# Performance work log

Measured on AMD Instinct MI355X. Metric: run time of the kernel, lower is better.

The kernel has to match this reference:

```python
import jax, jax.numpy as jnp
import numpy as np

G, S, P = 128, 32, 16          # graphs, subgraphs per graph, nodes per subgraph
D, C, NH, OUT = 768, 256, 4, 7 # input dim, hidden dim, GAT heads, classes


def setup_inputs() -> dict:
    key = jax.random.key(0)
    ks = jax.random.split(key, 17)
    n = lambda k, shape, s=0.05: jax.random.normal(k, shape, dtype=jnp.float32) * s
    return {
        "x": jax.random.normal(ks[0], (G, S, P, D), dtype=jnp.float32),
        # GATConv(768 -> 256, heads=4, concat=False): lin weight, att vectors, bias
        "gat_W": n(ks[1], (D, NH * C)),
        "att_src": n(ks[2], (NH, C)),
        "att_dst": n(ks[3], (NH, C)),
        "gat_b": n(ks[4], (C,)),
        # GRU(256 -> 256), torch layout [3*H, in]
        "gru_Wih": n(ks[5], (3 * C, C)),
        "gru_Whh": n(ks[6], (3 * C, C)),
        "gru_bih": n(ks[7], (3 * C,)),
        "gru_bhh": n(ks[8], (3 * C,)),
        # scale_up_projection Linear(256 -> 768)
        "up_W": n(ks[9], (D, C)),
        "up_b": n(ks[10], (D,)),
        # speaker_projection Linear(1536 -> 768) + ReLU
        "sp_W": n(ks[11], (D, 2 * D)),
        "sp_b": n(ks[12], (D,)),
        # GlobalAttention gate Linear(256 -> 1)
        "att_W": n(ks[13], (1, C)),
        "att_b": n(ks[14], (1,)),
        # classifier Linear(256 -> 7)
        "cls_W": n(ks[15], (OUT, C)),
        "cls_b": n(ks[16], (OUT,)),
    }


def _gat(x, W, a_src, a_dst, b):
    # PyG GATConv on a star graph (speaker = local node 0 -> all others) with
    # default add_self_loops=True, negative_slope=0.2, concat=False (mean over heads).
    # x: [G, P, D]
    h = jnp.einsum('gpd,dhc->gphc', x, W.reshape(D, NH, C))     # per-head transform
    es = jnp.sum(h * a_src, -1)                                 # [G, P, NH]
    ed = jnp.sum(h * a_dst, -1)
    lrelu = lambda v: jnp.where(v > 0, v, 0.2 * v)
    e_spk = lrelu(es[:, :1] + ed)   # edge speaker -> t
    e_slf = lrelu(es + ed)          # self loop t -> t
    w = jax.nn.softmax(jnp.stack([e_spk, e_slf], -1), axis=-1)  # [G, P, NH, 2]
    # for t == 0 both terms are h[:,0] and weights sum to 1, matching the
    # speaker node receiving only its self loop.
    out = w[..., 0:1] * h[:, :1] + w[..., 1:2] * h              # [G, P, NH, C]
    return out.mean(axis=2) + b


def _gru_cell(xin, h, Wih, Whh, bih, bhh):
    gi = xin @ Wih.T + bih
    gh = h @ Whh.T + bhh
    ir, iz, inn = jnp.split(gi, 3, -1)
    hr, hz, hn = jnp.split(gh, 3, -1)
    r = jax.nn.sigmoid(ir + hr)
    z = jax.nn.sigmoid(iz + hz)
    return (1 - z) * jnp.tanh(inn + r * hn) + z * h


def _forward(x, gat_W, att_src, att_dst, gat_b, gru_Wih, gru_Whh, gru_bih, gru_bhh,
             up_W, up_b, sp_W, sp_b, att_W, att_b, cls_W, cls_b):
    g, s, p, d = x.shape
    m0 = _gat(x[:, 0], gat_W, att_src, att_dst, gat_b)  # [G, P, C]
    h0 = jnp.zeros((g, p, C), x.dtype)

    def step(carry, _):
        h_run, m_prev = carry
        # running GRU hidden over memory prefix, then one zero-input step
        # (equivalent to rerunning the GRU over [m_0..m_{j-1}, 0])
        h_run = _gru_cell(m_prev, h_run, gru_Wih, gru_Whh, gru_bih, gru_bhh)
        h_nxt = _gru_cell(jnp.zeros_like(h_run), h_run, gru_Wih, gru_Whh, gru_bih, gru_bhh)
        pooled = h_nxt @ up_W.T + up_b                  # [G, P, D]
        # faithful to source: non_speaker_indices covers ALL nodes (torch.equal
        # shape-mismatch bug), and speaker_info is read AFTER the overwrite,
        # so the speaker concat is [pooled, pooled] and raw x[:, j>=1] is unused.
        spk = jnp.concatenate([pooled[:, 0], pooled[:, 0]], -1)  # [G, 2D]
        spk = jax.nn.relu(spk @ sp_W.T + sp_b)
        x_new = pooled.at[:, 0].set(spk)
        m = _gat(x_new, gat_W, att_src, att_dst, gat_b)
        return (h_run, m), m

    (_, _), ms = jax.lax.scan(step, (h0, m0), None, length=s - 1)
    mem = jnp.concatenate([m0[None], ms], axis=0)        # [S, G, P, C]
    # GlobalAttention pool over the P nodes of each subgraph memory state
    gate = jax.nn.softmax(jnp.squeeze(mem @ att_W.T + att_b, -1), axis=-1)  # [S, G, P]
    pooled = jnp.einsum('sgp,sgpc->sgc', gate, mem)
    logits = pooled @ cls_W.T + cls_b                    # [S, G, OUT]
    # torch stacks graph-major: [G*S, 1, OUT]
    return jnp.transpose(logits, (1, 0, 2)).reshape(g * s, 1, OUT)


def reference(x, gat_W, att_src, att_dst, gat_b, gru_Wih, gru_Whh, gru_bih, gru_bhh,
              up_W, up_b, sp_W, sp_b, att_W, att_b, cls_W, cls_b):
    return _forward(x, gat_W, att_src, att_dst, gat_b, gru_Wih, gru_Whh, gru_bih,
                    gru_bhh, up_W, up_b, sp_W, sp_b, att_W, att_b, cls_W, cls_b)
```

## Files before the change

### kernel.cpp

```cpp
#include <hip/hip_runtime.h>
#include <math.h>

#define NG 128
#define NS 32
#define NP 16
#define ND 768
#define NC 256
#define NHD 4
#define NOUT 7
#define NR 2048

typedef unsigned short ushortT;
typedef short bf16x8 __attribute__((ext_vector_type(8)));
typedef float f32x4 __attribute__((ext_vector_type(4)));

__device__ __forceinline__ ushortT f2b(float f) {
    union { float f; unsigned u; } v; v.f = f;
    unsigned r = (v.u + 0x7FFF + ((v.u >> 16) & 1)) >> 16;
    return (ushortT)r;
}
__device__ __forceinline__ float sigf(float v) { return 1.f / (1.f + expf(-v)); }

#define MFMA16(a, b, c) __builtin_amdgcn_mfma_f32_16x16x32_bf16((a), (b), (c), 0, 0, 0)

__global__ __launch_bounds__(256) void bgemm_kernel(
    const ushortT* __restrict__ A, const ushortT* __restrict__ Asub,
    const ushortT* __restrict__ Bt, const float* __restrict__ bias,
    float* __restrict__ outF, ushortT* __restrict__ outH,
    int N, int K, int act)
{
    __shared__ short As[64 * 40];
    __shared__ short Bs[64 * 40];
    const int tid = threadIdx.x;
    const int lane = tid & 63, wid = tid >> 6;
    const int quad = lane >> 4, l15 = lane & 15;
    const int row0 = blockIdx.y * 64, col0 = blockIdx.x * 64;
    const int mh = (wid & 1) * 32, nh = (wid >> 1) * 32;
    const int sr = tid >> 2, skq = (tid & 3) * 8;
    const int grow_s = row0 + sr;
    const ushortT* aptr = (Asub && ((grow_s & 15) == 0))
        ? Asub + (size_t)(grow_s >> 4) * K : A + (size_t)grow_s * K;
    const ushortT* bptr = Bt + (size_t)(col0 + sr) * K;

    f32x4 acc[2][2];
    for (int i = 0; i < 2; ++i)
        for (int j = 0; j < 2; ++j) acc[i][j] = (f32x4){0.f, 0.f, 0.f, 0.f};

    for (int kk = 0; kk < K; kk += 32) {
        __syncthreads();
        *(uint4*)&As[sr * 40 + skq] = *(const uint4*)(aptr + kk + skq);
        *(uint4*)&Bs[sr * 40 + skq] = *(const uint4*)(bptr + kk + skq);
        __syncthreads();
        bf16x8 af0 = *(const bf16x8*)&As[(mh + l15) * 40 + quad * 8];
        bf16x8 af1 = *(const bf16x8*)&As[(mh + 16 + l15) * 40 + quad * 8];
        bf16x8 bf0 = *(const bf16x8*)&Bs[(nh + l15) * 40 + quad * 8];
        bf16x8 bf1 = *(const bf16x8*)&Bs[(nh + 16 + l15) * 40 + quad * 8];
        acc[0][0] = MFMA16(af0, bf0, acc[0][0]);
        acc[0][1] = MFMA16(af0, bf1, acc[0][1]);
        acc[1][0] = MFMA16(af1, bf0, acc[1][0]);
        acc[1][1] = MFMA16(af1, bf1, acc[1][1]);
    }
#pragma unroll
    for (int mt = 0; mt < 2; ++mt)
#pragma unroll
        for (int nt = 0; nt < 2; ++nt) {
            const int gc = col0 + nh + nt * 16 + l15;
            const float bv = bias ? bias[gc] : 0.f;
#pragma unroll
            for (int r = 0; r < 4; ++r) {
                const int gr = row0 + mh + mt * 16 + quad * 4 + r;
                float v = acc[mt][nt][r] + bv;
                if (act) v = fmaxf(v, 0.f);
                if (outF) outF[(size_t)gr * N + gc] = v;
                if (outH) outH[(size_t)gr * N + gc] = f2b(v);
            }
        }
}

__global__ __launch_bounds__(256) void gru1_mfma_kernel(
    const ushortT* __restrict__ mB, const ushortT* __restrict__ hB,
    const ushortT* __restrict__ WihB, const ushortT* __restrict__ WhhB,
    const float* __restrict__ bih, const float* __restrict__ bhh,
    float* __restrict__ hF, ushortT* __restrict__ hBout)
{
    __shared__ short As[2 * 32 * 264];
    __shared__ short Bs[384 * 40];
    const int tid = threadIdx.x;
    const int lane = tid & 63, wid = tid >> 6;
    const int quad = lane >> 4, l15 = lane & 15;
    const int row0 = blockIdx.y * 32;
    const int n0 = blockIdx.x * 64;
    const int mt = wid & 1, nhh = (wid >> 1) * 32;

    for (int c = tid; c < 2048; c += 256) {
        const int mat = c >> 10, r2 = c & 1023, row = r2 >> 5, kc = (r2 & 31) * 8;
        const ushortT* src = (mat ? hB : mB) + (size_t)(row0 + row) * NC + kc;
        *(uint4*)&As[mat * 8448 + row * 264 + kc] = *(const uint4*)src;
    }
    f32x4 acc[2][3][2];
    for (int w = 0; w < 2; ++w)
        for (int g = 0; g < 3; ++g)
            for (int n = 0; n < 2; ++n) acc[w][g][n] = (f32x4){0.f, 0.f, 0.f, 0.f};

    for (int kk = 0; kk < 256; kk += 32) {
        __syncthreads();
        for (int c = tid; c < 1536; c += 256) {
            const int j = c >> 2, kq = (c & 3) * 8;
            const int w = j / 192, j2 = j - w * 192, gt = j2 >> 6, nloc = j2 & 63;
            const ushortT* src = (w ? WhhB : WihB) +
                (size_t)(gt * 256 + n0 + nloc) * NC + kk + kq;
            *(uint4*)&Bs[j * 40 + kq] = *(const uint4*)src;
        }
        __syncthreads();
        bf16x8 af0 = *(const bf16x8*)&As[(mt * 16 + l15) * 264 + kk + quad * 8];
        bf16x8 af1 = *(const bf16x8*)&As[8448 + (mt * 16 + l15) * 264 + kk + quad * 8];
#pragma unroll
        for (int gt = 0; gt < 3; ++gt)
#pragma unroll
            for (int nt = 0; nt < 2; ++nt) {
                const int jb = gt * 64 + nhh + nt * 16 + l15;
                bf16x8 b0 = *(const bf16x8*)&Bs[jb * 40 + quad * 8];
                bf16x8 b1 = *(const bf16x8*)&Bs[(192 + jb) * 40 + quad * 8];
                acc[0][gt][nt] = MFMA16(af0, b0, acc[0][gt][nt]);
                acc[1][gt][nt] = MFMA16(af1, b1, acc[1][gt][nt]);
            }
    }
#pragma unroll
    for (int nt = 0; nt < 2; ++nt) {
        const int c = n0 + nhh + nt * 16 + l15;
        const float br = bih[c], bz = bih[256 + c], bn = bih[512 + c];
        const float cr = bhh[c], cz = bhh[256 + c], cn = bhh[512 + c];
#pragma unroll
        for (int r = 0; r < 4; ++r) {
            const int grow = row0 + mt * 16 + quad * 4 + r;
            const size_t idx = (size_t)grow * NC + c;
            const float hold = hF[idx];
            const float rg = sigf(acc[0][0][nt][r] + br + acc[1][0][nt][r] + cr);
            const float zg = sigf(acc[0][1][nt][r] + bz + acc[1][1][nt][r] + cz);
            const float ng = tanhf(acc[0][2][nt][r] + bn + rg * (acc[1][2][nt][r] + cn));
            const float hn = (1.f - zg) * ng + zg * hold;
            hF[idx] = hn;
            hBout[idx] = f2b(hn);
        }
    }
}

__global__ __launch_bounds__(256) void gru2_mfma_kernel(
    const ushortT* __restrict__ hB, const ushortT* __restrict__ WhhB,
    const float* __restrict__ bih, const float* __restrict__ bhh,
    const float* __restrict__ hF, ushortT* __restrict__ hnB,
    ushortT* __restrict__ h0c)
{
    __shared__ short As[32 * 264];
    __shared__ short Bs[192 * 40];
    const int tid = threadIdx.x;
    const int lane = tid & 63, wid = tid >> 6;
    const int quad = lane >> 4, l15 = lane & 15;
    const int row0 = blockIdx.y * 32;
    const int n0 = blockIdx.x * 64;
    const int mt = wid & 1, nhh = (wid >> 1) * 32;

    for (int c = tid; c < 1024; c += 256) {
        const int row = c >> 5, kc = (c & 31) * 8;
        *(uint4*)&As[row * 264 + kc] =
            *(const uint4*)(hB + (size_t)(row0 + row) * NC + kc);
    }
    f32x4 acc[3][2];
    for (int g = 0; g < 3; ++g)
        for (int n = 0; n < 2; ++n) acc[g][n] = (f32x4){0.f, 0.f, 0.f, 0.f};

    for (int kk = 0; kk < 256; kk += 32) {
        __syncthreads();
        for (int c = tid; c < 768; c += 256) {
            const int j = c >> 2, kq = (c & 3) * 8;
            const int gt = j >> 6, nloc = j & 63;
            *(uint4*)&Bs[j * 40 + kq] =
                *(const uint4*)(WhhB + (size_t)(gt * 256 + n0 + nloc) * NC + kk + kq);
        }
        __syncthreads();
        bf16x8 af = *(const bf16x8*)&As[(mt * 16 + l15) * 264 + kk + quad * 8];
#pragma unroll
        for (int gt = 0; gt < 3; ++gt)
#pragma unroll
            for (int nt = 0; nt < 2; ++nt) {
                const int jb = gt * 64 + nhh + nt * 16 + l15;
                bf16x8 b = *(const bf16x8*)&Bs[jb * 40 + quad * 8];
                acc[gt][nt] = MFMA16(af, b, acc[gt][nt]);
            }
    }
#pragma unroll
    for (int nt = 0; nt < 2; ++nt) {
        const int c = n0 + nhh + nt * 16 + l15;
        const float br = bih[c], bz = bih[256 + c], bn = bih[512 + c];
        const float cr = bhh[c], cz = bhh[256 + c], cn = bhh[512 + c];
#pragma unroll
        for (int r = 0; r < 4; ++r) {
            const int grow = row0 + mt * 16 + quad * 4 + r;
            const size_t idx = (size_t)grow * NC + c;
            const float rg = sigf(br + acc[0][nt][r] + cr);
            const float zg = sigf(bz + acc[1][nt][r] + cz);
            const float ng = tanhf(bn + rg * (acc[2][nt][r] + cn));
            const float hv = (1.f - zg) * ng + zg * hF[idx];
            const ushortT hb = f2b(hv);
            hnB[idx] = hb;
            if ((grow & 15) == 0) h0c[(size_t)(grow >> 4) * NC + c] = hb;
        }
    }
}

__global__ __launch_bounds__(256) void fin_kernel(
    const float* __restrict__ hbuf, const float* __restrict__ att_src,
    const float* __restrict__ att_dst, const float* __restrict__ gat_b,
    const float* __restrict__ attW, const float* __restrict__ attb,
    const float* __restrict__ clsW, const float* __restrict__ clsb,
    ushortT* __restrict__ mB, float* __restrict__ outp, int s)
{
    const int g = blockIdx.x, tid = threadIdx.x;
    const int lane = tid & 63, wid = tid >> 6;
    __shared__ float es_s[16][4], ed_s[16][4];
    __shared__ float m_s[16][260];
    __shared__ float gate_s[16];
    __shared__ float pooled_s[256];
    const float* hb = hbuf + (size_t)g * NP * (NHD * NC);

    for (int pi = 0; pi < 4; ++pi) {
        const int p = wid * 4 + pi;
        const float* row = hb + p * (NHD * NC);
        float ss[4] = {0.f, 0.f, 0.f, 0.f}, sd[4] = {0.f, 0.f, 0.f, 0.f};
#pragma unroll
        for (int i = 0; i < 16; ++i) {
            const int col = lane + 64 * i;
            const float v = row[col];
            ss[i >> 2] += v * att_src[col];
            sd[i >> 2] += v * att_dst[col];
        }
        for (int off = 32; off; off >>= 1)
#pragma unroll
            for (int h = 0; h < 4; ++h) {
                ss[h] += __shfl_down(ss[h], off);
                sd[h] += __shfl_down(sd[h], off);
            }
        if (lane == 0)
#pragma unroll
            for (int h = 0; h < 4; ++h) { es_s[p][h] = ss[h]; ed_s[p][h] = sd[h]; }
    }
    __syncthreads();
    {
        const int p = tid >> 4, cb = (tid & 15) * 16;
        float accv[16];
#pragma unroll
        for (int cj = 0; cj < 16; ++cj) accv[cj] = 0.f;
#pragma unroll
        for (int h = 0; h < 4; ++h) {
            float e1 = es_s[0][h] + ed_s[p][h]; e1 = e1 > 0.f ? e1 : 0.2f * e1;
            float e2 = es_s[p][h] + ed_s[p][h]; e2 = e2 > 0.f ? e2 : 0.2f * e2;
            const float mx = fmaxf(e1, e2);
            float w0 = expf(e1 - mx), w1 = expf(e2 - mx);
            const float inv = 1.f / (w0 + w1);
            w0 *= inv; w1 *= inv;
            const float* r0 = hb + h * NC + cb;
            const float* rp = hb + p * (NHD * NC) + h * NC + cb;
#pragma unroll
            for (int cj = 0; cj < 16; ++cj) accv[cj] += w0 * r0[cj] + w1 * rp[cj];
        }
#pragma unroll
        for (int cj = 0; cj < 16; ++cj) {
            const float v = accv[cj] * 0.25f + gat_b[cb + cj];
            m_s[p][cb + cj] = v;
            mB[(size_t)(g * NP + p) * NC + cb + cj] = f2b(v);
        }
    }
    __syncthreads();
    for (int pi = 0; pi < 4; ++pi) {
        const int p = wid * 4 + pi;
        float sg = 0.f;
#pragma unroll
        for (int i = 0; i < 4; ++i) { const int c = lane + 64 * i; sg += m_s[p][c] * attW[c]; }
        for (int off = 32; off; off >>= 1) sg += __shfl_down(sg, off);
        if (lane == 0) gate_s[p] = sg + attb[0];
    }
    __syncthreads();
    float mx = -1e30f;
#pragma unroll
    for (int p = 0; p < 16; ++p) mx = fmaxf(mx, gate_s[p]);
    float ge[16], ssum = 0.f;
#pragma unroll
    for (int p = 0; p < 16; ++p) { ge[p] = expf(gate_s[p] - mx); ssum += ge[p]; }
    const float inv = 1.f / ssum;
    {
        float pc = 0.f;
#pragma unroll
        for (int p = 0; p < 16; ++p) pc += ge[p] * m_s[p][tid];
        pooled_s[tid] = pc * inv;
    }
    __syncthreads();
    const int o = tid >> 5, l32 = tid & 31;
    if (o < NOUT) {
        float a = 0.f;
#pragma unroll
        for (int i = 0; i < 8; ++i) {
            const int c = l32 + 32 * i;
            a += pooled_s[c] * clsW[o * NC + c];
        }
        for (int off = 16; off; off >>= 1) a += __shfl_down(a, off);
        if (l32 == 0) outp[((size_t)g * NS + s) * NOUT + o] = a + clsb[o];
    }
}

__global__ __launch_bounds__(256) void cast_kernel(const float* __restrict__ a,
                                                   ushortT* __restrict__ b, int n) {
    const int i = blockIdx.x * 256 + threadIdx.x;
    if (i < n) b[i] = f2b(a[i]);
}
__global__ __launch_bounds__(256) void gatT_kernel(const float* __restrict__ gW,
                                                   ushortT* __restrict__ gB) {
    const int idx = blockIdx.x * 256 + threadIdx.x;
    const int c = idx / ND, d = idx - c * ND;
    gB[idx] = f2b(gW[(size_t)d * (NHD * NC) + c]);
}
__global__ __launch_bounds__(256) void spwc_kernel(const float* __restrict__ spW,
                                                   float* __restrict__ o) {
    const int idx = blockIdx.x * 256 + threadIdx.x;
    const int r = idx / ND, d = idx - r * ND;
    o[idx] = spW[(size_t)r * (2 * ND) + d] + spW[(size_t)r * (2 * ND) + ND + d];
}
__global__ __launch_bounds__(256) void wus_kernel(const float* __restrict__ spWc,
                                                  const float* __restrict__ upW,
                                                  ushortT* __restrict__ WusB) {
    const int c = threadIdx.x;
    const int o0 = blockIdx.x * 16;
    float acc[16];
#pragma unroll
    for (int i = 0; i < 16; ++i) acc[i] = 0.f;
    for (int d = 0; d < ND; ++d) {
        const float u = upW[(size_t)d * NC + c];
#pragma unroll
        for (int i = 0; i < 16; ++i) acc[i] += spWc[(size_t)(o0 + i) * ND + d] * u;
    }
#pragma unroll
    for (int i = 0; i < 16; ++i) WusB[(size_t)(o0 + i) * NC + c] = f2b(acc[i]);
}
__global__ __launch_bounds__(256) void bus_kernel(const float* __restrict__ spWc,
                                                  const float* __restrict__ up_b,
                                                  const float* __restrict__ sp_b,
                                                  float* __restrict__ bus) {
    const int o = blockIdx.x * 256 + threadIdx.x;
    if (o >= ND) return;
    float a = sp_b[o];
    const float* sr = spWc + (size_t)o * ND;
    for (int d = 0; d < ND; ++d) a += sr[d] * up_b[d];
    bus[o] = a;
}
__global__ __launch_bounds__(256) void x0_kernel(const float* __restrict__ x,
                                                 ushortT* __restrict__ xb) {
    const int idx = blockIdx.x * 256 + threadIdx.x;
    const int row = idx / ND, d = idx - row * ND;
    const int g = row >> 4, p = row & 15;
    xb[idx] = f2b(x[((size_t)g * (NS * NP) + p) * ND + d]);
}
__global__ __launch_bounds__(256) void zh_kernel(float* hF, ushortT* hB) {
    const int idx = blockIdx.x * 256 + threadIdx.x;
    hF[idx] = 0.f;
    hB[idx] = 0;
}

extern "C" void kernel_launch(void* const* d_in, const int* in_sizes, int n_in,
                              void* d_out, int out_size, void* d_ws, size_t ws_size,
                              hipStream_t stream) {
    (void)in_sizes; (void)n_in; (void)out_size; (void)ws_size;
    const float* x       = (const float*)d_in[0];
    const float* gat_W   = (const float*)d_in[1];
    const float* att_src = (const float*)d_in[2];
    const float* att_dst = (const float*)d_in[3];
    const float* gat_b   = (const float*)d_in[4];
    const float* gru_Wih = (const float*)d_in[5];
    const float* gru_Whh = (const float*)d_in[6];
    const float* gru_bih = (const float*)d_in[7];
    const float* gru_bhh = (const float*)d_in[8];
    const float* up_W    = (const float*)d_in[9];
    const float* up_b    = (const float*)d_in[10];
    const float* sp_W    = (const float*)d_in[11];
    const float* sp_b    = (const float*)d_in[12];
    const float* att_W   = (const float*)d_in[13];
    const float* att_b   = (const float*)d_in[14];
    const float* cls_W   = (const float*)d_in[15];
    const float* cls_b   = (const float*)d_in[16];
    float* outp = (float*)d_out;

    char* w = (char*)d_ws;
    ushortT* xb    = (ushortT*)w; w += (size_t)NR * ND * 2;
    ushortT* WihB  = (ushortT*)w; w += (size_t)(3 * NC) * NC * 2;
    ushortT* WhhB  = (ushortT*)w; w += (size_t)(3 * NC) * NC * 2;
    ushortT* upWB  = (ushortT*)w; w += (size_t)ND * NC * 2;
    ushortT* gatB  = (ushortT*)w; w += (size_t)(NHD * NC) * ND * 2;
    ushortT* WusB  = (ushortT*)w; w += (size_t)ND * NC * 2;
    float*   spWc  = (float*)w;   w += (size_t)ND * ND * 4;
    float*   bus   = (float*)w;   w += (size_t)ND * 4;
    float*   hF    = (float*)w;   w += (size_t)NR * NC * 4;
    ushortT* hB    = (ushortT*)w; w += (size_t)NR * NC * 2;
    ushortT* hnB   = (ushortT*)w; w += (size_t)NR * NC * 2;
    ushortT* h0c   = (ushortT*)w; w += (size_t)NG * NC * 2;
    ushortT* poolB = (ushortT*)w; w += (size_t)NR * ND * 2;
    ushortT* spkB  = (ushortT*)w; w += (size_t)NG * ND * 2;
    float*   hbuf  = (float*)w;   w += (size_t)NR * (NHD * NC) * 4;
    ushortT* mB    = (ushortT*)w; w += (size_t)NR * NC * 2;

    cast_kernel<<<768, 256, 0, stream>>>(gru_Wih, WihB, 3 * NC * NC);
    cast_kernel<<<768, 256, 0, stream>>>(gru_Whh, WhhB, 3 * NC * NC);
    cast_kernel<<<768, 256, 0, stream>>>(up_W, upWB, ND * NC);
    gatT_kernel<<<(NHD * NC * ND) / 256, 256, 0, stream>>>(gat_W, gatB);
    spwc_kernel<<<(ND * ND) / 256, 256, 0, stream>>>(sp_W, spWc);
    wus_kernel<<<ND / 16, 256, 0, stream>>>(spWc, up_W, WusB);
    bus_kernel<<<3, 256, 0, stream>>>(spWc, up_b, sp_b, bus);
    x0_kernel<<<(NR * ND) / 256, 256, 0, stream>>>(x, xb);
    zh_kernel<<<(NR * NC) / 256, 256, 0, stream>>>(hF, hB);

    bgemm_kernel<<<dim3((NHD * NC) / 64, NR / 64), 256, 0, stream>>>(
        xb, nullptr, gatB, nullptr, hbuf, nullptr, NHD * NC, ND, 0);
    fin_kernel<<<NG, 256, 0, stream>>>(hbuf, att_src, att_dst, gat_b,
                                       att_W, att_b, cls_W, cls_b, mB, outp, 0);

    for (int j = 1; j < NS; ++j) {
        gru1_mfma_kernel<<<dim3(NC / 64, NR / 32), 256, 0, stream>>>(
            mB, hB, WihB, WhhB, gru_bih, gru_bhh, hF, hB);
        gru2_mfma_kernel<<<dim3(NC / 64, NR / 32), 256, 0, stream>>>(
            hB, WhhB, gru_bih, gru_bhh, hF, hnB, h0c);
        bgemm_kernel<<<dim3(ND / 64, NR / 64), 256, 0, stream>>>(
            hnB, nullptr, upWB, up_b, nullptr, poolB, ND, NC, 0);
        bgemm_kernel<<<dim3(ND / 64, NG / 64), 256, 0, stream>>>(
            h0c, nullptr, WusB, bus, nullptr, spkB, ND, NC, 1);
        bgemm_kernel<<<dim3((NHD * NC) / 64, NR / 64), 256, 0, stream>>>(
            poolB, spkB, gatB, nullptr, hbuf, nullptr, NHD * NC, ND, 0);
        fin_kernel<<<NG, 256, 0, stream>>>(hbuf, att_src, att_dst, gat_b,
                                           att_W, att_b, cls_W, cls_b, mB, outp, j);
    }
}
```

Measured before the change: 2.644 ms.

## Fuse whole recurrent scan into one persistent per-graph kernel with folded up-projection

Measured after the change: 5.463 ms. +106.6%, slower.

```diff
diff --git a/kernel.cpp b/kernel.cpp
--- a/kernel.cpp
+++ b/kernel.cpp
@@ -8,7 +8,6 @@
 #define NC 256
 #define NHD 4
 #define NOUT 7
-#define NR 2048
 
 typedef unsigned short ushortT;
 typedef short bf16x8 __attribute__((ext_vector_type(8)));
@@ -19,15 +18,17 @@
     unsigned r = (v.u + 0x7FFF + ((v.u >> 16) & 1)) >> 16;
     return (ushortT)r;
 }
+__device__ __forceinline__ float b2f(ushortT u) {
+    union { unsigned u; float f; } v; v.u = ((unsigned)u) << 16; return v.f;
+}
 __device__ __forceinline__ float sigf(float v) { return 1.f / (1.f + expf(-v)); }
 
 #define MFMA16(a, b, c) __builtin_amdgcn_mfma_f32_16x16x32_bf16((a), (b), (c), 0, 0, 0)
+#define ZERO4 ((f32x4){0.f, 0.f, 0.f, 0.f})
 
 __global__ __launch_bounds__(256) void bgemm_kernel(
-    const ushortT* __restrict__ A, const ushortT* __restrict__ Asub,
-    const ushortT* __restrict__ Bt, const float* __restrict__ bias,
-    float* __restrict__ outF, ushortT* __restrict__ outH,
-    int N, int K, int act)
+    const ushortT* __restrict__ A, const ushortT* __restrict__ Bt,
+    ushortT* __restrict__ outH, int N, int K)
 {
     __shared__ short As[64 * 40];
     __shared__ short Bs[64 * 40];
@@ -37,15 +38,10 @@
     const int row0 = blockIdx.y * 64, col0 = blockIdx.x * 64;
     const int mh = (wid & 1) * 32, nh = (wid >> 1) * 32;
     const int sr = tid >> 2, skq = (tid & 3) * 8;
-    const int grow_s = row0 + sr;
-    const ushortT* aptr = (Asub && ((grow_s & 15) == 0))
-        ? Asub + (size_t)(grow_s >> 4) * K : A + (size_t)grow_s * K;
+    const ushortT* aptr = A + (size_t)(row0 + sr) * K;
     const ushortT* bptr = Bt + (size_t)(col0 + sr) * K;
 
-    f32x4 acc[2][2];
-    for (int i = 0; i < 2; ++i)
-        for (int j = 0; j < 2; ++j) acc[i][j] = (f32x4){0.f, 0.f, 0.f, 0.f};
-
+    f32x4 acc[2][2] = {{ZERO4, ZERO4}, {ZERO4, ZERO4}};
     for (int kk = 0; kk < K; kk += 32) {
         __syncthreads();
         *(uint4*)&As[sr * 40 + skq] = *(const uint4*)(aptr + kk + skq);
@@ -65,246 +61,12 @@
 #pragma unroll
         for (int nt = 0; nt < 2; ++nt) {
             const int gc = col0 + nh + nt * 16 + l15;
-            const float bv = bias ? bias[gc] : 0.f;
 #pragma unroll
             for (int r = 0; r < 4; ++r) {
                 const int gr = row0 + mh + mt * 16 + quad * 4 + r;
-                float v = acc[mt][nt][r] + bv;
-                if (act) v = fmaxf(v, 0.f);
-                if (outF) outF[(size_t)gr * N + gc] = v;
-                if (outH) outH[(size_t)gr * N + gc] = f2b(v);
-            }
-        }
-}
-
-__global__ __launch_bounds__(256) void gru1_mfma_kernel(
-    const ushortT* __restrict__ mB, const ushortT* __restrict__ hB,
-    const ushortT* __restrict__ WihB, const ushortT* __restrict__ WhhB,
-    const float* __restrict__ bih, const float* __restrict__ bhh,
-    float* __restrict__ hF, ushortT* __restrict__ hBout)
-{
-    __shared__ short As[2 * 32 * 264];
-    __shared__ short Bs[384 * 40];
-    const int tid = threadIdx.x;
-    const int lane = tid & 63, wid = tid >> 6;
-    const int quad = lane >> 4, l15 = lane & 15;
-    const int row0 = blockIdx.y * 32;
-    const int n0 = blockIdx.x * 64;
-    const int mt = wid & 1, nhh = (wid >> 1) * 32;
-
-    for (int c = tid; c < 2048; c += 256) {
-        const int mat = c >> 10, r2 = c & 1023, row = r2 >> 5, kc = (r2 & 31) * 8;
-        const ushortT* src = (mat ? hB : mB) + (size_t)(row0 + row) * NC + kc;
-        *(uint4*)&As[mat * 8448 + row * 264 + kc] = *(const uint4*)src;
-    }
-    f32x4 acc[2][3][2];
-    for (int w = 0; w < 2; ++w)
-        for (int g = 0; g < 3; ++g)
-            for (int n = 0; n < 2; ++n) acc[w][g][n] = (f32x4){0.f, 0.f, 0.f, 0.f};
-
-    for (int kk = 0; kk < 256; kk += 32) {
-        __syncthreads();
-        for (int c = tid; c < 1536; c += 256) {
-            const int j = c >> 2, kq = (c & 3) * 8;
-            const int w = j / 192, j2 = j - w * 192, gt = j2 >> 6, nloc = j2 & 63;
-            const ushortT* src = (w ? WhhB : WihB) +
-                (size_t)(gt * 256 + n0 + nloc) * NC + kk + kq;
-            *(uint4*)&Bs[j * 40 + kq] = *(const uint4*)src;
-        }
-        __syncthreads();
-        bf16x8 af0 = *(const bf16x8*)&As[(mt * 16 + l15) * 264 + kk + quad * 8];
-        bf16x8 af1 = *(const bf16x8*)&As[8448 + (mt * 16 + l15) * 264 + kk + quad * 8];
-#pragma unroll
-        for (int gt = 0; gt < 3; ++gt)
-#pragma unroll
-            for (int nt = 0; nt < 2; ++nt) {
-                const int jb = gt * 64 + nhh + nt * 16 + l15;
-                bf16x8 b0 = *(const bf16x8*)&Bs[jb * 40 + quad * 8];
-                bf16x8 b1 = *(const bf16x8*)&Bs[(192 + jb) * 40 + quad * 8];
-                acc[0][gt][nt] = MFMA16(af0, b0, acc[0][gt][nt]);
-                acc[1][gt][nt] = MFMA16(af1, b1, acc[1][gt][nt]);
-            }
-    }
-#pragma unroll
-    for (int nt = 0; nt < 2; ++nt) {
-        const int c = n0 + nhh + nt * 16 + l15;
-        const float br = bih[c], bz = bih[256 + c], bn = bih[512 + c];
-        const float cr = bhh[c], cz = bhh[256 + c], cn = bhh[512 + c];
-#pragma unroll
-        for (int r = 0; r < 4; ++r) {
-            const int grow = row0 + mt * 16 + quad * 4 + r;
-            const size_t idx = (size_t)grow * NC + c;
-            const float hold = hF[idx];
-            const float rg = sigf(acc[0][0][nt][r] + br + acc[1][0][nt][r] + cr);
-            const float zg = sigf(acc[0][1][nt][r] + bz + acc[1][1][nt][r] + cz);
-            const float ng = tanhf(acc[0][2][nt][r] + bn + rg * (acc[1][2][nt][r] + cn));
-            const float hn = (1.f - zg) * ng + zg * hold;
-            hF[idx] = hn;
-            hBout[idx] = f2b(hn);
-        }
-    }
-}
-
-__global__ __launch_bounds__(256) void gru2_mfma_kernel(
-    const ushortT* __restrict__ hB, const ushortT* __restrict__ WhhB,
-    const float* __restrict__ bih, const float* __restrict__ bhh,
-    const float* __restrict__ hF, ushortT* __restrict__ hnB,
-    ushortT* __restrict__ h0c)
-{
-    __shared__ short As[32 * 264];
-    __shared__ short Bs[192 * 40];
-    const int tid = threadIdx.x;
-    const int lane = tid & 63, wid = tid >> 6;
-    const int quad = lane >> 4, l15 = lane & 15;
-    const int row0 = blockIdx.y * 32;
-    const int n0 = blockIdx.x * 64;
-    const int mt = wid & 1, nhh = (wid >> 1) * 32;
-
-    for (int c = tid; c < 1024; c += 256) {
-        const int row = c >> 5, kc = (c & 31) * 8;
-        *(uint4*)&As[row * 264 + kc] =
-            *(const uint4*)(hB + (size_t)(row0 + row) * NC + kc);
-    }
-    f32x4 acc[3][2];
-    for (int g = 0; g < 3; ++g)
-        for (int n = 0; n < 2; ++n) acc[g][n] = (f32x4){0.f, 0.f, 0.f, 0.f};
-
-    for (int kk = 0; kk < 256; kk += 32) {
-        __syncthreads();
-        for (int c = tid; c < 768; c += 256) {
-            const int j = c >> 2, kq = (c & 3) * 8;
-            const int gt = j >> 6, nloc = j & 63;
-            *(uint4*)&Bs[j * 40 + kq] =
-                *(const uint4*)(WhhB + (size_t)(gt * 256 + n0 + nloc) * NC + kk + kq);
-        }
-        __syncthreads();
-        bf16x8 af = *(const bf16x8*)&As[(mt * 16 + l15) * 264 + kk + quad * 8];
-#pragma unroll
-        for (int gt = 0; gt < 3; ++gt)
-#pragma unroll
-            for (int nt = 0; nt < 2; ++nt) {
-                const int jb = gt * 64 + nhh + nt * 16 + l15;
-                bf16x8 b = *(const bf16x8*)&Bs[jb * 40 + quad * 8];
-                acc[gt][nt] = MFMA16(af, b, acc[gt][nt]);
-            }
-    }
-#pragma unroll
-    for (int nt = 0; nt < 2; ++nt) {
-        const int c = n0 + nhh + nt * 16 + l15;
-        const float br = bih[c], bz = bih[256 + c], bn = bih[512 + c];
-        const float cr = bhh[c], cz = bhh[256 + c], cn = bhh[512 + c];
-#pragma unroll
-        for (int r = 0; r < 4; ++r) {
-            const int grow = row0 + mt * 16 + quad * 4 + r;
-            const size_t idx = (size_t)grow * NC + c;
-            const float rg = sigf(br + acc[0][nt][r] + cr);
-            const float zg = sigf(bz + acc[1][nt][r] + cz);
-            const float ng = tanhf(bn + rg * (acc[2][nt][r] + cn));
-            const float hv = (1.f - zg) * ng + zg * hF[idx];
-            const ushortT hb = f2b(hv);
-            hnB[idx] = hb;
-            if ((grow & 15) == 0) h0c[(size_t)(grow >> 4) * NC + c] = hb;
-        }
-    }
-}
-
-__global__ __launch_bounds__(256) void fin_kernel(
-    const float* __restrict__ hbuf, const float* __restrict__ att_src,
-    const float* __restrict__ att_dst, const float* __restrict__ gat_b,
-    const float* __restrict__ attW, const float* __restrict__ attb,
-    const float* __restrict__ clsW, const float* __restrict__ clsb,
-    ushortT* __restrict__ mB, float* __restrict__ outp, int s)
-{
-    const int g = blockIdx.x, tid = threadIdx.x;
-    const int lane = tid & 63, wid = tid >> 6;
-    __shared__ float es_s[16][4], ed_s[16][4];
-    __shared__ float m_s[16][260];
-    __shared__ float gate_s[16];
-    __shared__ float pooled_s[256];
-    const float* hb = hbuf + (size_t)g * NP * (NHD * NC);
-
-    for (int pi = 0; pi < 4; ++pi) {
-        const int p = wid * 4 + pi;
-        const float* row = hb + p * (NHD * NC);
-        float ss[4] = {0.f, 0.f, 0.f, 0.f}, sd[4] = {0.f, 0.f, 0.f, 0.f};
-#pragma unroll
-        for (int i = 0; i < 16; ++i) {
-            const int col = lane + 64 * i;
-            const float v = row[col];
-            ss[i >> 2] += v * att_src[col];
-            sd[i >> 2] += v * att_dst[col];
-        }
-        for (int off = 32; off; off >>= 1)
-#pragma unroll
-            for (int h = 0; h < 4; ++h) {
-                ss[h] += __shfl_down(ss[h], off);
-                sd[h] += __shfl_down(sd[h], off);
-            }
-        if (lane == 0)
-#pragma unroll
-            for (int h = 0; h < 4; ++h) { es_s[p][h] = ss[h]; ed_s[p][h] = sd[h]; }
-    }
-    __syncthreads();
-    {
-        const int p = tid >> 4, cb = (tid & 15) * 16;
-        float accv[16];
-#pragma unroll
-        for (int cj = 0; cj < 16; ++cj) accv[cj] = 0.f;
-#pragma unroll
-        for (int h = 0; h < 4; ++h) {
-            float e1 = es_s[0][h] + ed_s[p][h]; e1 = e1 > 0.f ? e1 : 0.2f * e1;
-            float e2 = es_s[p][h] + ed_s[p][h]; e2 = e2 > 0.f ? e2 : 0.2f * e2;
-            const float mx = fmaxf(e1, e2);
-            float w0 = expf(e1 - mx), w1 = expf(e2 - mx);
-            const float inv = 1.f / (w0 + w1);
-            w0 *= inv; w1 *= inv;
-            const float* r0 = hb + h * NC + cb;
-            const float* rp = hb + p * (NHD * NC) + h * NC + cb;
-#pragma unroll
-            for (int cj = 0; cj < 16; ++cj) accv[cj] += w0 * r0[cj] + w1 * rp[cj];
-        }
-#pragma unroll
-        for (int cj = 0; cj < 16; ++cj) {
-            const float v = accv[cj] * 0.25f + gat_b[cb + cj];
-            m_s[p][cb + cj] = v;
-            mB[(size_t)(g * NP + p) * NC + cb + cj] = f2b(v);
-        }
-    }
-    __syncthreads();
-    for (int pi = 0; pi < 4; ++pi) {
-        const int p = wid * 4 + pi;
-        float sg = 0.f;
-#pragma unroll
-        for (int i = 0; i < 4; ++i) { const int c = lane + 64 * i; sg += m_s[p][c] * attW[c]; }
-        for (int off = 32; off; off >>= 1) sg += __shfl_down(sg, off);
-        if (lane == 0) gate_s[p] = sg + attb[0];
-    }
-    __syncthreads();
-    float mx = -1e30f;
-#pragma unroll
-    for (int p = 0; p < 16; ++p) mx = fmaxf(mx, gate_s[p]);
-    float ge[16], ssum = 0.f;
-#pragma unroll
-    for (int p = 0; p < 16; ++p) { ge[p] = expf(gate_s[p] - mx); ssum += ge[p]; }
-    const float inv = 1.f / ssum;
-    {
-        float pc = 0.f;
-#pragma unroll
-        for (int p = 0; p < 16; ++p) pc += ge[p] * m_s[p][tid];
-        pooled_s[tid] = pc * inv;
-    }
-    __syncthreads();
-    const int o = tid >> 5, l32 = tid & 31;
-    if (o < NOUT) {
-        float a = 0.f;
-#pragma unroll
-        for (int i = 0; i < 8; ++i) {
-            const int c = l32 + 32 * i;
-            a += pooled_s[c] * clsW[o * NC + c];
-        }
-        for (int off = 16; off; off >>= 1) a += __shfl_down(a, off);
-        if (l32 == 0) outp[((size_t)g * NS + s) * NOUT + o] = a + clsb[o];
-    }
+                outH[(size_t)gr * N + gc] = f2b(acc[mt][nt][r]);
+            }
+        }
 }
 
 __global__ __launch_bounds__(256) void cast_kernel(const float* __restrict__ a,
@@ -318,50 +80,307 @@
     const int c = idx / ND, d = idx - c * ND;
     gB[idx] = f2b(gW[(size_t)d * (NHD * NC) + c]);
 }
-__global__ __launch_bounds__(256) void spwc_kernel(const float* __restrict__ spW,
-                                                   float* __restrict__ o) {
+__global__ __launch_bounds__(256) void spwcB_kernel(const float* __restrict__ spW,
+                                                    ushortT* __restrict__ o) {
     const int idx = blockIdx.x * 256 + threadIdx.x;
     const int r = idx / ND, d = idx - r * ND;
-    o[idx] = spW[(size_t)r * (2 * ND) + d] + spW[(size_t)r * (2 * ND) + ND + d];
-}
-__global__ __launch_bounds__(256) void wus_kernel(const float* __restrict__ spWc,
-                                                  const float* __restrict__ upW,
-                                                  ushortT* __restrict__ WusB) {
-    const int c = threadIdx.x;
-    const int o0 = blockIdx.x * 16;
-    float acc[16];
-#pragma unroll
-    for (int i = 0; i < 16; ++i) acc[i] = 0.f;
-    for (int d = 0; d < ND; ++d) {
-        const float u = upW[(size_t)d * NC + c];
-#pragma unroll
-        for (int i = 0; i < 16; ++i) acc[i] += spWc[(size_t)(o0 + i) * ND + d] * u;
-    }
-#pragma unroll
-    for (int i = 0; i < 16; ++i) WusB[(size_t)(o0 + i) * NC + c] = f2b(acc[i]);
-}
-__global__ __launch_bounds__(256) void bus_kernel(const float* __restrict__ spWc,
+    o[idx] = f2b(spW[(size_t)r * (2 * ND) + d] + spW[(size_t)r * (2 * ND) + ND + d]);
+}
+__global__ __launch_bounds__(256) void upTc_kernel(const float* __restrict__ upW,
+                                                   ushortT* __restrict__ o) {
+    const int idx = blockIdx.x * 256 + threadIdx.x;
+    if (idx >= NC * ND) return;
+    const int c = idx / ND, d = idx - c * ND;
+    o[idx] = f2b(upW[(size_t)d * NC + c]);
+}
+__global__ __launch_bounds__(256) void bus_kernel(const float* __restrict__ spW,
                                                   const float* __restrict__ up_b,
                                                   const float* __restrict__ sp_b,
                                                   float* __restrict__ bus) {
     const int o = blockIdx.x * 256 + threadIdx.x;
     if (o >= ND) return;
     float a = sp_b[o];
-    const float* sr = spWc + (size_t)o * ND;
-    for (int d = 0; d < ND; ++d) a += sr[d] * up_b[d];
+    const float* sr = spW + (size_t)o * (2 * ND);
+    for (int d = 0; d < ND; ++d) a += (sr[d] + sr[ND + d]) * up_b[d];
     bus[o] = a;
 }
-__global__ __launch_bounds__(256) void x0_kernel(const float* __restrict__ x,
-                                                 ushortT* __restrict__ xb) {
-    const int idx = blockIdx.x * 256 + threadIdx.x;
-    const int row = idx / ND, d = idx - row * ND;
-    const int g = row >> 4, p = row & 15;
-    xb[idx] = f2b(x[((size_t)g * (NS * NP) + p) * ND + d]);
-}
-__global__ __launch_bounds__(256) void zh_kernel(float* hF, ushortT* hB) {
-    const int idx = blockIdx.x * 256 + threadIdx.x;
-    hF[idx] = 0.f;
-    hB[idx] = 0;
+__global__ __launch_bounds__(256) void bug_kernel(const ushortT* __restrict__ gatB,
+                                                  const float* __restrict__ up_b,
+                                                  float* __restrict__ bug) {
+    const int col = blockIdx.x * 256 + threadIdx.x;
+    float a = 0.f;
+    const ushortT* gr = gatB + (size_t)col * ND;
+    for (int d = 0; d < ND; ++d) a += b2f(gr[d]) * up_b[d];
+    bug[col] = a;
+}
+
+__global__ __launch_bounds__(1024) void iter_kernel(
+    const float* __restrict__ x,
+    const ushortT* __restrict__ gatB,
+    const ushortT* __restrict__ WihB,
+    const ushortT* __restrict__ WhhB,
+    const ushortT* __restrict__ WusB,
+    const ushortT* __restrict__ WugT,
+    const float* __restrict__ bus,
+    const float* __restrict__ bug,
+    const float* __restrict__ bih, const float* __restrict__ bhh,
+    const float* __restrict__ att_src, const float* __restrict__ att_dst,
+    const float* __restrict__ gat_b,
+    const float* __restrict__ attW, const float* __restrict__ attb,
+    const float* __restrict__ clsW, const float* __restrict__ clsb,
+    float* __restrict__ outp)
+{
+    __shared__ short mB_s[16 * 264];
+    __shared__ short hB_s[16 * 264];
+    __shared__ short hn_s[16 * 264];
+    __shared__ float hF_s[16 * 264];
+    __shared__ float msf[16 * 264];
+    __shared__ short hb_s[16 * 1040];
+    __shared__ short spk_s[776];
+    __shared__ float es_s[64], ed_s[64];
+    __shared__ float gate_s[16];
+    __shared__ float pooled_s[256];
+
+    const int g = blockIdx.x;
+    const int tid = threadIdx.x;
+    const int lane = tid & 63, wid = tid >> 6;
+    const int quad = lane >> 4, l15 = lane & 15;
+
+    for (int i = tid; i < 16 * 264; i += 1024) { hF_s[i] = 0.f; hB_s[i] = 0; }
+    __syncthreads();
+
+    int ct[4];
+#pragma unroll
+    for (int t = 0; t < 4; ++t) ct[t] = ((wid * 4 + t) << 4) + l15;
+
+    {
+        const float* xrow = x + ((size_t)g * NS * NP + l15) * ND;
+        f32x4 acc[4] = {ZERO4, ZERO4, ZERO4, ZERO4};
+        for (int kk = 0; kk < ND; kk += 32) {
+            const float4 xa = *(const float4*)(xrow + kk + quad * 8);
+            const float4 xb2 = *(const float4*)(xrow + kk + quad * 8 + 4);
+            bf16x8 a;
+            a[0] = (short)f2b(xa.x); a[1] = (short)f2b(xa.y);
+            a[2] = (short)f2b(xa.z); a[3] = (short)f2b(xa.w);
+            a[4] = (short)f2b(xb2.x); a[5] = (short)f2b(xb2.y);
+            a[6] = (short)f2b(xb2.z); a[7] = (short)f2b(xb2.w);
+#pragma unroll
+            for (int t = 0; t < 4; ++t) {
+                bf16x8 b = *(const bf16x8*)(gatB + (size_t)ct[t] * ND + kk + quad * 8);
+                acc[t] = MFMA16(a, b, acc[t]);
+            }
+        }
+#pragma unroll
+        for (int t = 0; t < 4; ++t)
+#pragma unroll
+            for (int r = 0; r < 4; ++r)
+                hb_s[(quad * 4 + r) * 1040 + ct[t]] = (short)f2b(acc[t][r]);
+    }
+    __syncthreads();
+
+    const int c_own = (wid << 4) + l15;
+
+    for (int s = 0; s < NS; ++s) {
+        {
+            const int p = wid;
+            float ss[4] = {0.f, 0.f, 0.f, 0.f}, sd[4] = {0.f, 0.f, 0.f, 0.f};
+#pragma unroll
+            for (int i = 0; i < 16; ++i) {
+                const int col = lane + (i << 6);
+                const float v = b2f((ushortT)hb_s[p * 1040 + col]);
+                ss[i >> 2] += v * att_src[col];
+                sd[i >> 2] += v * att_dst[col];
+            }
+            for (int off = 32; off; off >>= 1)
+#pragma unroll
+                for (int h = 0; h < 4; ++h) {
+                    ss[h] += __shfl_down(ss[h], off);
+                    sd[h] += __shfl_down(sd[h], off);
+                }
+            if (lane == 0)
+#pragma unroll
+                for (int h = 0; h < 4; ++h) { es_s[p * 4 + h] = ss[h]; ed_s[p * 4 + h] = sd[h]; }
+        }
+        __syncthreads();
+        {
+            const int p = tid >> 6, c0 = lane << 2;
+            float accv[4] = {0.f, 0.f, 0.f, 0.f};
+#pragma unroll
+            for (int h = 0; h < 4; ++h) {
+                float e1 = es_s[h] + ed_s[p * 4 + h];
+                e1 = e1 > 0.f ? e1 : 0.2f * e1;
+                float e2 = es_s[p * 4 + h] + ed_s[p * 4 + h];
+                e2 = e2 > 0.f ? e2 : 0.2f * e2;
+                const float mx = fmaxf(e1, e2);
+                float w0 = expf(e1 - mx), w1 = expf(e2 - mx);
+                const float inv = 1.f / (w0 + w1);
+                w0 *= inv; w1 *= inv;
+#pragma unroll
+                for (int j = 0; j < 4; ++j) {
+                    const int col = h * NC + c0 + j;
+                    accv[j] += w0 * b2f((ushortT)hb_s[col])
+                             + w1 * b2f((ushortT)hb_s[p * 1040 + col]);
+                }
+            }
+#pragma unroll
+            for (int j = 0; j < 4; ++j) {
+                const float v = accv[j] * 0.25f + gat_b[c0 + j];
+                msf[p * 264 + c0 + j] = v;
+                mB_s[p * 264 + c0 + j] = (short)f2b(v);
+            }
+        }
+        __syncthreads();
+        {
+            const int p = wid;
+            float sg = 0.f;
+#pragma unroll
+            for (int i = 0; i < 4; ++i) {
+                const int c = lane + (i << 6);
+                sg += msf[p * 264 + c] * attW[c];
+            }
+            for (int off = 32; off; off >>= 1) sg += __shfl_down(sg, off);
+            if (lane == 0) gate_s[p] = sg + attb[0];
+        }
+        __syncthreads();
+        if (tid < NC) {
+            float mx = gate_s[0];
+#pragma unroll
+            for (int p = 1; p < 16; ++p) mx = fmaxf(mx, gate_s[p]);
+            float sum = 0.f, pc = 0.f;
+#pragma unroll
+            for (int p = 0; p < 16; ++p) {
+                const float e = expf(gate_s[p] - mx);
+                sum += e;
+                pc += e * msf[p * 264 + tid];
+            }
+            pooled_s[tid] = pc / sum;
+        }
+        __syncthreads();
+        if (wid < NOUT) {
+            float a = 0.f;
+#pragma unroll
+            for (int i = 0; i < 4; ++i) {
+                const int c = lane + (i << 6);
+                a += pooled_s[c] * clsW[wid * NC + c];
+            }
+            for (int off = 32; off; off >>= 1) a += __shfl_down(a, off);
+            if (lane == 0) outp[((size_t)g * NS + s) * NOUT + wid] = a + clsb[wid];
+        }
+        if (s == NS - 1) break;
+
+        {
+            const ushortT* bi = WihB + (size_t)c_own * NC + quad * 8;
+            const ushortT* bh = WhhB + (size_t)c_own * NC + quad * 8;
+            f32x4 agi[3] = {ZERO4, ZERO4, ZERO4};
+            f32x4 agh[3] = {ZERO4, ZERO4, ZERO4};
+            for (int kk = 0; kk < NC; kk += 32) {
+                bf16x8 am = *(const bf16x8*)&mB_s[l15 * 264 + kk + quad * 8];
+                bf16x8 ah = *(const bf16x8*)&hB_s[l15 * 264 + kk + quad * 8];
+#pragma unroll
+                for (int gt = 0; gt < 3; ++gt) {
+                    bf16x8 wi = *(const bf16x8*)(bi + gt * 65536 + kk);
+                    bf16x8 wh = *(const bf16x8*)(bh + gt * 65536 + kk);
+                    agi[gt] = MFMA16(am, wi, agi[gt]);
+                    agh[gt] = MFMA16(ah, wh, agh[gt]);
+                }
+            }
+            __syncthreads();
+            const float br = bih[c_own], bz = bih[NC + c_own], bn = bih[2 * NC + c_own];
+            const float cr = bhh[c_own], cz = bhh[NC + c_own], cn = bhh[2 * NC + c_own];
+#pragma unroll
+            for (int r = 0; r < 4; ++r) {
+                const int idx = (quad * 4 + r) * 264 + c_own;
+                const float hold = hF_s[idx];
+                const float rg = sigf(agi[0][r] + br + agh[0][r] + cr);
+                const float zg = sigf(agi[1][r] + bz + agh[1][r] + cz);
+                const float ng = tanhf(agi[2][r] + bn + rg * (agh[2][r] + cn));
+                const float hn = (1.f - zg) * ng + zg * hold;
+                hF_s[idx] = hn;
+                hB_s[idx] = (short)f2b(hn);
+            }
+        }
+        __syncthreads();
+
+        {
+            const ushortT* bh = WhhB + (size_t)c_own * NC + quad * 8;
+            f32x4 agh[3] = {ZERO4, ZERO4, ZERO4};
+            for (int kk = 0; kk < NC; kk += 32) {
+                bf16x8 ah = *(const bf16x8*)&hB_s[l15 * 264 + kk + quad * 8];
+#pragma unroll
+                for (int gt = 0; gt < 3; ++gt) {
+                    bf16x8 wh = *(const bf16x8*)(bh + gt * 65536 + kk);
+                    agh[gt] = MFMA16(ah, wh, agh[gt]);
+                }
+            }
+            const float br = bih[c_own], bz = bih[NC + c_own], bn = bih[2 * NC + c_own];
+            const float cr = bhh[c_own], cz = bhh[NC + c_own], cn = bhh[2 * NC + c_own];
+#pragma unroll
+            for (int r = 0; r < 4; ++r) {
+                const int idx = (quad * 4 + r) * 264 + c_own;
+                const float rg = sigf(br + agh[0][r] + cr);
+                const float zg = sigf(bz + agh[1][r] + cz);
+                const float ng = tanhf(bn + rg * (agh[2][r] + cn));
+                const float hv = (1.f - zg) * ng + zg * hF_s[idx];
+                hn_s[idx] = (short)f2b(hv);
+            }
+        }
+        __syncthreads();
+
+        if (tid < ND) {
+            float acc = bus[tid];
+            const ushortT* wrow = WusB + (size_t)tid * NC;
+            for (int k = 0; k < NC; k += 8) {
+                bf16x8 hv = *(const bf16x8*)&hn_s[k];
+                bf16x8 wv = *(const bf16x8*)(wrow + k);
+#pragma unroll
+                for (int j = 0; j < 8; ++j)
+                    acc += b2f((ushortT)hv[j]) * b2f((ushortT)wv[j]);
+            }
+            spk_s[tid] = (short)f2b(fmaxf(acc, 0.f));
+        }
+        __syncthreads();
+
+        {
+            f32x4 acc[4] = {ZERO4, ZERO4, ZERO4, ZERO4};
+            for (int kk = 0; kk < NC; kk += 32) {
+                bf16x8 a = *(const bf16x8*)&hn_s[l15 * 264 + kk + quad * 8];
+#pragma unroll
+                for (int t = 0; t < 4; ++t) {
+                    bf16x8 b = *(const bf16x8*)(WugT + (size_t)ct[t] * NC + kk + quad * 8);
+                    acc[t] = MFMA16(a, b, acc[t]);
+                }
+            }
+#pragma unroll
+            for (int t = 0; t < 4; ++t) {
+                const float bv = bug[ct[t]];
+#pragma unroll
+                for (int r = 0; r < 4; ++r) {
+                    const int row = quad * 4 + r;
+                    if (row != 0)
+                        hb_s[row * 1040 + ct[t]] = (short)f2b(acc[t][r] + bv);
+                }
+            }
+        }
+        {
+            f32x4 acc[4] = {ZERO4, ZERO4, ZERO4, ZERO4};
+            for (int kk = 0; kk < ND; kk += 32) {
+                bf16x8 a;
+                if (l15 == 0) a = *(const bf16x8*)&spk_s[kk + quad * 8];
+                else a = (bf16x8){0, 0, 0, 0, 0, 0, 0, 0};
+#pragma unroll
+                for (int t = 0; t < 4; ++t) {
+                    bf16x8 b = *(const bf16x8*)(gatB + (size_t)ct[t] * ND + kk + quad * 8);
+                    acc[t] = MFMA16(a, b, acc[t]);
+                }
+            }
+            if (quad == 0) {
+#pragma unroll
+                for (int t = 0; t < 4; ++t)
+                    hb_s[ct[t]] = (short)f2b(acc[t][0]);
+            }
+        }
+        __syncthreads();
+    }
 }
 
 extern "C" void kernel_launch(void* const* d_in, const int* in_sizes, int n_in,
@@ -388,50 +407,30 @@
     float* outp = (float*)d_out;
 
     char* w = (char*)d_ws;
-    ushortT* xb    = (ushortT*)w; w += (size_t)NR * ND * 2;
     ushortT* WihB  = (ushortT*)w; w += (size_t)(3 * NC) * NC * 2;
     ushortT* WhhB  = (ushortT*)w; w += (size_t)(3 * NC) * NC * 2;
-    ushortT* upWB  = (ushortT*)w; w += (size_t)ND * NC * 2;
     ushortT* gatB  = (ushortT*)w; w += (size_t)(NHD * NC) * ND * 2;
+    ushortT* spwcB = (ushortT*)w; w += (size_t)ND * ND * 2;
+    ushortT* upWTc = (ushortT*)w; w += (size_t)NC * ND * 2;
     ushortT* WusB  = (ushortT*)w; w += (size_t)ND * NC * 2;
-    float*   spWc  = (float*)w;   w += (size_t)ND * ND * 4;
+    ushortT* WugT  = (ushortT*)w; w += (size_t)(NHD * NC) * NC * 2;
     float*   bus   = (float*)w;   w += (size_t)ND * 4;
-    float*   hF    = (float*)w;   w += (size_t)NR * NC * 4;
-    ushortT* hB    = (ushortT*)w; w += (size_t)NR * NC * 2;
-    ushortT* hnB   = (ushortT*)w; w += (size_t)NR * NC * 2;
-    ushortT* h0c   = (ushortT*)w; w += (size_t)NG * NC * 2;
-    ushortT* poolB = (ushortT*)w; w += (size_t)NR * ND * 2;
-    ushortT* spkB  = (ushortT*)w; w += (size_t)NG * ND * 2;
-    float*   hbuf  = (float*)w;   w += (size_t)NR * (NHD * NC) * 4;
-    ushortT* mB    = (ushortT*)w; w += (size_t)NR * NC * 2;
+    float*   bug   = (float*)w;   w += (size_t)(NHD * NC) * 4;
 
     cast_kernel<<<768, 256, 0, stream>>>(gru_Wih, WihB, 3 * NC * NC);
     cast_kernel<<<768, 256, 0, stream>>>(gru_Whh, WhhB, 3 * NC * NC);
-    cast_kernel<<<768, 256, 0, stream>>>(up_W, upWB, ND * NC);
     gatT_kernel<<<(NHD * NC * ND) / 256, 256, 0, stream>>>(gat_W, gatB);
-    spwc_kernel<<<(ND * ND) / 256, 256, 0, stream>>>(sp_W, spWc);
-    wus_kernel<<<ND / 16, 256, 0, stream>>>(spWc, up_W, WusB);
-    bus_kernel<<<3, 256, 0, stream>>>(spWc, up_b, sp_b, bus);
-    x0_kernel<<<(NR * ND) / 256, 256, 0, stream>>>(x, xb);
-    zh_kernel<<<(NR * NC) / 256, 256, 0, stream>>>(hF, hB);
-
-    bgemm_kernel<<<dim3((NHD * NC) / 64, NR / 64), 256, 0, stream>>>(
-        xb, nullptr, gatB, nullptr, hbuf, nullptr, NHD * NC, ND, 0);
-    fin_kernel<<<NG, 256, 0, stream>>>(hbuf, att_src, att_dst, gat_b,
-                                       att_W, att_b, cls_W, cls_b, mB, outp, 0);
-
-    for (int j = 1; j < NS; ++j) {
-        gru1_mfma_kernel<<<dim3(NC / 64, NR / 32), 256, 0, stream>>>(
-            mB, hB, WihB, WhhB, gru_bih, gru_bhh, hF, hB);
-        gru2_mfma_kernel<<<dim3(NC / 64, NR / 32), 256, 0, stream>>>(
-            hB, WhhB, gru_bih, gru_bhh, hF, hnB, h0c);
-        bgemm_kernel<<<dim3(ND / 64, NR / 64), 256, 0, stream>>>(
-            hnB, nullptr, upWB, up_b, nullptr, poolB, ND, NC, 0);
-        bgemm_kernel<<<dim3(ND / 64, NG / 64), 256, 0, stream>>>(
-            h0c, nullptr, WusB, bus, nullptr, spkB, ND, NC, 1);
-        bgemm_kernel<<<dim3((NHD * NC) / 64, NR / 64), 256, 0, stream>>>(
-            poolB, spkB, gatB, nullptr, hbuf, nullptr, NHD * NC, ND, 0);
-        fin_kernel<<<NG, 256, 0, stream>>>(hbuf, att_src, att_dst, gat_b,
-                                           att_W, att_b, cls_W, cls_b, mB, outp, j);
-    }
-}
+    spwcB_kernel<<<(ND * ND) / 256, 256, 0, stream>>>(sp_W, spwcB);
+    upTc_kernel<<<(NC * ND) / 256, 256, 0, stream>>>(up_W, upWTc);
+    bgemm_kernel<<<dim3(NC / 64, ND / 64), 256, 0, stream>>>(
+        spwcB, upWTc, WusB, NC, ND);
+    bgemm_kernel<<<dim3(NC / 64, (NHD * NC) / 64), 256, 0, stream>>>(
+        gatB, upWTc, WugT, NC, ND);
+    bus_kernel<<<3, 256, 0, stream>>>(sp_W, up_b, sp_b, bus);
+    bug_kernel<<<4, 256, 0, stream>>>(gatB, up_b, bug);
+
+    iter_kernel<<<NG, 1024, 0, stream>>>(
+        x, gatB, WihB, WhhB, WusB, WugT, bus, bug,
+        gru_bih, gru_bhh, att_src, att_dst, gat_b,
+        att_W, att_b, cls_W, cls_b, outp);
+}
```
